# Performance work log

Measured on AMD Instinct MI355X. Metric: run time of the kernel, lower is better.

The kernel has to match this reference:

```python
import jax, jax.numpy as jnp
import numpy as np

B, S, R = 8, 4096, 512
E, K, ATOMS, XAR, TOPK = 64, 256, 16, 3, 2
TEMP = 1.0


def setup_inputs() -> dict:
    key = jax.random.key(0)
    k0, k1, k2, k3, k4 = jax.random.split(key, 5)
    x_latent = jax.random.normal(k0, (B, S, R), jnp.float32)
    router_w = jax.random.normal(k1, (E, R), jnp.float32) * (1.0 / np.sqrt(R))
    atoms = jax.random.normal(k2, (E, ATOMS, R), jnp.float32) * 0.01
    combo_weights = jax.random.uniform(k3, (E, K, XAR), jnp.float32) * 0.5 + 0.25
    combo_logits = jax.random.normal(k4, (E, K, XAR, ATOMS), jnp.float32) * 0.01
    return {"x_latent": x_latent, "router_w": router_w, "atoms": atoms,
            "combo_weights": combo_weights, "combo_logits": combo_logits}


def _expert_centroids(atoms, combo_weights, combo_logits):
    # Hard codeword path (vectorized over experts):
    # sign atoms -> pick argmax atom per (k, xor slot) -> weight -> sum -> sign -> mean over k
    binary = jnp.sign(atoms)                                   # [E, A, R]
    # softmax(logits/t) then argmax == argmax(logits) (monotone)
    idx = jnp.argmax(combo_logits, axis=-1)                    # [E, K, XAR]
    sel = binary[jnp.arange(E)[:, None, None], idx]            # [E, K, XAR, R]
    codewords = jnp.sign((sel * combo_weights[..., None]).sum(axis=2))  # [E, K, R]
    return codewords.mean(axis=1)                              # [E, R]


def reference(x_latent, router_w, atoms, combo_weights, combo_logits):
    t = max(TEMP, 0.1)
    router_logits = jnp.einsum('bsr,er->bse', x_latent, router_w)   # [B, S, E]
    probs_t = jax.nn.softmax(router_logits / t, axis=-1)
    gates, expert_ids = jax.lax.top_k(probs_t, TOPK)                # [B, S, 2]
    gates = gates / gates.sum(axis=-1, keepdims=True)

    centroids = _expert_centroids(atoms, combo_weights, combo_logits)  # [E, R]

    # aux load-balancing loss (uses untempered softmax)
    router_prob = jax.nn.softmax(router_logits, axis=-1)
    aux_loss = E * jnp.sum(router_prob.mean(axis=(0, 1)) *
                           (router_prob > 0).astype(x_latent.dtype).mean(axis=(0, 1)))

    # dense per-expert gate = sum over topk slots of gate * (id == e), then combine with centroids
    dense_gates = (jax.nn.one_hot(expert_ids, E, dtype=gates.dtype) *
                   gates[..., None]).sum(axis=-2)                    # [B, S, E]
    combined = jnp.einsum('bse,er->bsr', dense_gates, centroids)     # [B, S, R]
    return combined, aux_loss
```

## Files before the change

kernel.cpp:

```cpp
#include <hip/hip_runtime.h>
#include <math.h>

#define TOKENS 32768
#define RDIM 512
#define NEXP 64
#define NK 256
#define LDQ 136
#define PSTR 67
#define TAU 4.0e-3f

typedef unsigned short u16;
typedef float f32x4 __attribute__((ext_vector_type(4)));
typedef short s16x8 __attribute__((ext_vector_type(8)));

#define MFMA_B16(a, b, c) __builtin_amdgcn_mfma_f32_16x16x32_bf16(a, b, c, 0, 0, 0)

__device__ __forceinline__ void split_pack(float4 v, unsigned& h01, unsigned& h23,
                                           unsigned& l01, unsigned& l23) {
    unsigned u0 = __float_as_uint(v.x), u1 = __float_as_uint(v.y);
    unsigned u2 = __float_as_uint(v.z), u3 = __float_as_uint(v.w);
    float r0 = v.x - __uint_as_float(u0 & 0xFFFF0000u);
    float r1 = v.y - __uint_as_float(u1 & 0xFFFF0000u);
    float r2 = v.z - __uint_as_float(u2 & 0xFFFF0000u);
    float r3 = v.w - __uint_as_float(u3 & 0xFFFF0000u);
    h01 = (u0 >> 16) | (u1 & 0xFFFF0000u);
    h23 = (u2 >> 16) | (u3 & 0xFFFF0000u);
    l01 = (__float_as_uint(r0) >> 16) | (__float_as_uint(r1) & 0xFFFF0000u);
    l23 = (__float_as_uint(r2) >> 16) | (__float_as_uint(r3) & 0xFFFF0000u);
}

__device__ __forceinline__ void split8(float4 a, float4 b, s16x8& hi, s16x8& lo) {
    union U { unsigned u[4]; s16x8 v; };
    U H, L;
    split_pack(a, H.u[0], H.u[1], L.u[0], L.u[1]);
    split_pack(b, H.u[2], H.u[3], L.u[2], L.u[3]);
    hi = H.v; lo = L.v;
}

__global__ __launch_bounds__(256) void centroid_kernel(
    const float* __restrict__ atoms,
    const float* __restrict__ cw,
    const float* __restrict__ cl,
    float* __restrict__ cent,
    float* __restrict__ aux_sum,
    unsigned* __restrict__ aux_cnt)
{
    __shared__ unsigned pack[NK];
    const int e    = blockIdx.x >> 1;
    const int half = blockIdx.x & 1;
    const int tid  = threadIdx.x;

    if (blockIdx.x == 0 && tid < 64) { aux_sum[tid] = 0.f; aux_cnt[tid] = 0u; }

    {
        const int k = tid;
        unsigned u = 0;
        float w3[3];
        #pragma unroll
        for (int xx = 0; xx < 3; ++xx) {
            const float* cp = cl + ((((size_t)e * NK + k) * 3 + xx) << 4);
            float v[16];
            *(float4*)(v + 0)  = *(const float4*)(cp + 0);
            *(float4*)(v + 4)  = *(const float4*)(cp + 4);
            *(float4*)(v + 8)  = *(const float4*)(cp + 8);
            *(float4*)(v + 12) = *(const float4*)(cp + 12);
            float best = v[0]; int bi = 0;
            #pragma unroll
            for (int a = 1; a < 16; ++a) {
                if (v[a] > best) { best = v[a]; bi = a; }
            }
            u |= (unsigned)bi << (4 * xx);
            w3[xx] = cw[((size_t)e * NK + k) * 3 + xx];
        }
        unsigned lut = 0;
        #pragma unroll
        for (int c = 0; c < 8; ++c) {
            float val = ((c & 1) ? -w3[0] : w3[0])
                      + ((c & 2) ? -w3[1] : w3[1])
                      + ((c & 4) ? -w3[2] : w3[2]);
            lut |= (val < 0.f ? 1u : 0u) << c;
        }
        pack[k] = u | (lut << 16);
    }

    const int r = half * 256 + tid;
    unsigned B0 = 0;
    #pragma unroll
    for (int a = 0; a < 16; ++a)
        B0 |= (atoms[((size_t)e * 16 + a) * RDIM + r] < 0.f ? 1u : 0u) << a;
    __syncthreads();

    int n0 = 0;
    #pragma unroll 2
    for (int k = 0; k < NK; k += 8) {
        unsigned pk[8];
        #pragma unroll
        for (int j = 0; j < 8; ++j) pk[j] = pack[k + j];
        #pragma unroll
        for (int j = 0; j < 8; ++j) {
            unsigned u  = pk[j];
            unsigned i0 = u & 15u, i1 = (u >> 4) & 15u, i2 = (u >> 8) & 15u;
            unsigned c0 = ((B0 >> i0) & 1u) | (((B0 >> i1) & 1u) << 1) | (((B0 >> i2) & 1u) << 2);
            n0 += (u >> (16 + c0)) & 1u;
        }
    }
    cent[(size_t)e * RDIM + r] = 1.f - (float)n0 * (1.f / 128.f);
}

__global__ __launch_bounds__(256, 4) void moe_main(
    const float* __restrict__ x,
    const float* __restrict__ w,
    const float* __restrict__ cent,
    float* __restrict__ out,
    float* __restrict__ aux_sum,
    unsigned* __restrict__ aux_cnt)
{
    __shared__ u16 wlds[2 * 64 * LDQ];
    u16* whi = wlds;
    u16* wlo = wlds + 64 * LDQ;
    float* P     = (float*)wlds;
    float* candv = P + 64 * PSTR;
    int*   candi = (int*)(candv + 64 * 13);
    float* qsum  = (float*)(candi + 64 * 13);
    float* gateL = qsum + 64 * 5;
    __shared__ float s_aux[64];
    __shared__ unsigned s_cnt[64];

    const int tid  = threadIdx.x;
    const int lane = tid & 63;
    const int wave = tid >> 6;
    const int l15  = lane & 15;
    const int kgrp = (lane >> 4) << 3;
    const int tok0 = blockIdx.x * 64;

    if (tid < 64) { s_aux[tid] = 0.f; s_cnt[tid] = 0u; }

    f32x4 acc[4];
    #pragma unroll
    for (int nt = 0; nt < 4; ++nt) acc[nt] = (f32x4){0.f, 0.f, 0.f, 0.f};

    const float* xlane = x + (size_t)(tok0 + wave * 16 + l15) * RDIM + kgrp;
    const int wrow = tid >> 2;
    const int wseg = tid & 3;
    const float* wg = w + (size_t)wrow * RDIM + wseg * 32;
    const int woff = wrow * LDQ + wseg * 32;

    float4 preA[4], preB[4];
    #pragma unroll
    for (int i = 0; i < 4; ++i) {
        preA[i] = *(const float4*)(xlane + i * 32);
        preB[i] = *(const float4*)(xlane + i * 32 + 4);
    }

    #pragma unroll
    for (int q = 0; q < 4; ++q) {
        if (q) __syncthreads();
        {
            const float* wq = wg + q * 128;
            uint2 h2[2], l2[2];
            #pragma unroll
            for (int j = 0; j < 8; ++j) {
                float4 wv = *(const float4*)(wq + j * 4);
                split_pack(wv, h2[j & 1].x, h2[j & 1].y, l2[j & 1].x, l2[j & 1].y);
                if (j & 1) {
                    *(uint4*)&whi[woff + (j - 1) * 4] =
                        make_uint4(h2[0].x, h2[0].y, h2[1].x, h2[1].y);
                    *(uint4*)&wlo[woff + (j - 1) * 4] =
                        make_uint4(l2[0].x, l2[0].y, l2[1].x, l2[1].y);
                }
            }
        }
        __syncthreads();

        #pragma unroll
        for (int kb = 0; kb < 4; ++kb) {
            const int g = q * 4 + kb;
            s16x8 ah, al;
            split8(preA[g & 3], preB[g & 3], ah, al);
            if (g + 4 < 16) {
                const float* nx = xlane + (g + 4) * 32;
                preA[g & 3] = *(const float4*)(nx);
                preB[g & 3] = *(const float4*)(nx + 4);
            }
            const int kl = kb * 32 + kgrp;
            #pragma unroll
            for (int nt = 0; nt < 4; ++nt) {
                const int brow = nt * 16 + l15;
                s16x8 bh = *(const s16x8*)&whi[brow * LDQ + kl];
                s16x8 bl = *(const s16x8*)&wlo[brow * LDQ + kl];
                acc[nt] = MFMA_B16(ah, bh, acc[nt]);
                acc[nt] = MFMA_B16(ah, bl, acc[nt]);
                acc[nt] = MFMA_B16(al, bh, acc[nt]);
            }
        }
    }

    __syncthreads();
    #pragma unroll
    for (int nt = 0; nt < 4; ++nt)
        #pragma unroll
        for (int i = 0; i < 4; ++i)
            P[(wave * 16 + ((lane >> 4) << 2) + i) * PSTR + nt * 16 + l15] = acc[nt][i];
    __syncthreads();

    const int tt = tid & 63;
    const int ss = tid >> 6;
    float v[16];
    #pragma unroll
    for (int j = 0; j < 16; ++j) v[j] = P[tt * PSTR + ss * 16 + j];

    float m1 = -INFINITY, m2 = -INFINITY, m3 = -INFINITY;
    int   i1 = NEXP, i2 = NEXP, i3 = NEXP;
    #pragma unroll
    for (int j = 0; j < 16; ++j) {
        float val = v[j]; int e = ss * 16 + j;
        if (val > m1)      { m3 = m2; i3 = i2; m2 = m1; i2 = i1; m1 = val; i1 = e; }
        else if (val > m2) { m3 = m2; i3 = i2; m2 = val; i2 = e; }
        else if (val > m3) { m3 = val; i3 = e; }
    }
    candv[tt * 13 + ss * 3 + 0] = m1; candi[tt * 13 + ss * 3 + 0] = i1;
    candv[tt * 13 + ss * 3 + 1] = m2; candi[tt * 13 + ss * 3 + 1] = i2;
    candv[tt * 13 + ss * 3 + 2] = m3; candi[tt * 13 + ss * 3 + 2] = i3;
    __syncthreads();

    m1 = m2 = m3 = -INFINITY; i1 = i2 = i3 = NEXP;
    #pragma unroll
    for (int q = 0; q < 12; ++q) {
        float val = candv[tt * 13 + q]; int e = candi[tt * 13 + q];
        if (val > m1)      { m3 = m2; i3 = i2; m2 = m1; i2 = i1; m1 = val; i1 = e; }
        else if (val > m2) { m3 = m2; i3 = i2; m2 = val; i2 = e; }
        else if (val > m3) { m3 = val; i3 = e; }
    }

    float ex[16]; float ps = 0.f;
    #pragma unroll
    for (int j = 0; j < 16; ++j) { ex[j] = __expf(v[j] - m1); ps += ex[j]; }
    qsum[tt * 5 + ss] = ps;

    if (ss == 0) {
        {
            const float ed  = __expf(m2 - m1);
            const float inv = 1.f / (1.f + ed);
            gateL[tt * 4 + 0] = inv;
            gateL[tt * 4 + 1] = ed * inv;
            ((int*)gateL)[tt * 4 + 2] = i1;
            ((int*)gateL)[tt * 4 + 3] = i2;
        }
        unsigned long long bmask = __ballot(m2 - m3 < TAU);
        while (bmask) {
            const int f = __ffsll(bmask) - 1;
            bmask &= bmask - 1;
            int id3[3];
            id3[0] = __shfl(i1, f); id3[1] = __shfl(i2, f); id3[2] = __shfl(i3, f);
            const float* xrow = x + (size_t)(tok0 + f) * RDIM + lane * 8;
            float4 a0 = *(const float4*)(xrow);
            float4 a1 = *(const float4*)(xrow + 4);
            float d[3];
            #pragma unroll
            for (int jj = 0; jj < 3; ++jj) {
                const float* wrow2 = w + (size_t)id3[jj] * RDIM + lane * 8;
                float4 b0 = *(const float4*)(wrow2);
                float4 b1 = *(const float4*)(wrow2 + 4);
                float p = a0.x * b0.x;
                p = fmaf(a0.y, b0.y, p); p = fmaf(a0.z, b0.z, p); p = fmaf(a0.w, b0.w, p);
                p = fmaf(a1.x, b1.x, p); p = fmaf(a1.y, b1.y, p);
                p = fmaf(a1.z, b1.z, p); p = fmaf(a1.w, b1.w, p);
                #pragma unroll
                for (int off = 32; off; off >>= 1) p += __shfl_xor(p, off);
                d[jj] = p;
            }
            int b = 0;
            if (d[1] > d[0] || (d[1] == d[0] && id3[1] < id3[0])) b = 1;
            if (d[2] > d[b] || (d[2] == d[b] && id3[2] < id3[b])) b = 2;
            int sec;
            if (b == 0)      sec = (d[1] > d[2] || (d[1] == d[2] && id3[1] < id3[2])) ? 1 : 2;
            else if (b == 1) sec = (d[0] > d[2] || (d[0] == d[2] && id3[0] < id3[2])) ? 0 : 2;
            else             sec = (d[0] > d[1] || (d[0] == d[1] && id3[0] < id3[1])) ? 0 : 1;
            if (lane == f) {
                const float ed  = __expf(d[sec] - d[b]);
                const float inv = 1.f / (1.f + ed);
                gateL[f * 4 + 0] = inv;
                gateL[f * 4 + 1] = ed * inv;
                ((int*)gateL)[f * 4 + 2] = id3[b];
                ((int*)gateL)[f * 4 + 3] = id3[sec];
            }
        }
    }
    __syncthreads();

    float Z = 0.f;
    #pragma unroll
    for (int k = 0; k < 4; ++k) Z += qsum[tt * 5 + k];
    const float invZ = 1.f / Z;
    #pragma unroll
    for (int j = 0; j < 16; ++j) P[tt * PSTR + ss * 16 + j] = ex[j] * invZ;
    __syncthreads();

    {
        const int e = tid & 63, tq = tid >> 6;
        float s = 0.f; unsigned cn = 0u;
        #pragma unroll
        for (int t = 0; t < 16; ++t) {
            float pv = P[(tq * 16 + t) * PSTR + e];
            s += pv; cn += (pv > 0.f) ? 1u : 0u;
        }
        atomicAdd(&s_aux[e], s);
        atomicAdd(&s_cnt[e], cn);
    }
    __syncthreads();
    if (tid < 64) {
        atomicAdd(aux_sum + tid, s_aux[tid]);
        atomicAdd(aux_cnt + tid, s_cnt[tid]);
    }

    {
        const int e = lane;
        #pragma unroll
        for (int s2 = 0; s2 < 16; ++s2) {
            const int t2 = wave * 16 + s2;
            float4 g4 = *(float4*)&gateL[t2 * 4];
            const float g1 = g4.x, g2 = g4.y;
            const int e1 = __float_as_int(g4.z), e2 = __float_as_int(g4.w);
            const float4* c1 = (const float4*)(cent + (size_t)e1 * RDIM);
            const float4* c2 = (const float4*)(cent + (size_t)e2 * RDIM);
            float4* op = (float4*)(out + (size_t)(tok0 + t2) * RDIM);
            float4 A0 = c1[e],      Bb0 = c2[e];
            float4 A1 = c1[e + 64], Bb1 = c2[e + 64];
            float4 o0, o1;
            o0.x = fmaf(g1, A0.x, g2 * Bb0.x); o0.y = fmaf(g1, A0.y, g2 * Bb0.y);
            o0.z = fmaf(g1, A0.z, g2 * Bb0.z); o0.w = fmaf(g1, A0.w, g2 * Bb0.w);
            o1.x = fmaf(g1, A1.x, g2 * Bb1.x); o1.y = fmaf(g1, A1.y, g2 * Bb1.y);
            o1.z = fmaf(g1, A1.z, g2 * Bb1.z); o1.w = fmaf(g1, A1.w, g2 * Bb1.w);
            op[e]      = o0;
            op[e + 64] = o1;
        }
    }
}

__global__ __launch_bounds__(64) void aux_kernel(
    const float* __restrict__ sums,
    const unsigned* __restrict__ cnts,
    float* __restrict__ out_aux)
{
    const int e = threadIdx.x;
    float v = (sums[e] * (1.f / (float)TOKENS)) * ((float)cnts[e] * (1.f / (float)TOKENS));
    #pragma unroll
    for (int off = 32; off; off >>= 1) v += __shfl_xor(v, off);
    if (e == 0) out_aux[0] = (float)NEXP * v;
}

extern "C" void kernel_launch(void* const* d_in, const int* in_sizes, int n_in,
                              void* d_out, int out_size, void* d_ws, size_t ws_size,
                              hipStream_t stream) {
    const float* x     = (const float*)d_in[0];
    const float* rw    = (const float*)d_in[1];
    const float* atoms = (const float*)d_in[2];
    const float* cwts  = (const float*)d_in[3];
    const float* clog  = (const float*)d_in[4];
    float* out = (float*)d_out;

    float*    aux_sum = (float*)d_ws;
    unsigned* aux_cnt = (unsigned*)((char*)d_ws + 256);
    float*    cent    = (float*)((char*)d_ws + 512);

    centroid_kernel<<<128, 256, 0, stream>>>(atoms, cwts, clog, cent, aux_sum, aux_cnt);
    moe_main<<<512, 256, 0, stream>>>(x, rw, cent, out, aux_sum, aux_cnt);
    aux_kernel<<<1, 64, 0, stream>>>(aux_sum, aux_cnt, out + (size_t)TOKENS * RDIM);
}
```

Measured before the change: 165.7 us.

## Pre-split router weights into MFMA fragment layout, add smaller-block fast path

Router weights are split into bf16 hi/lo once in a prep kernel, which runs alongside the centroid computation. They are stored in a layout that matches the MFMA B-fragment, so the main kernel loads them straight from global/L2 instead of re-splitting and staging them through LDS in every block. The main kernel now uses 128-thread blocks covering 32 tokens each, with a 1024-block grid and a smaller LDS footprint, which should allow higher occupancy and removes the per-quarter syncthreads. The fast path is chosen only when the workspace is large enough. It trades LDS reuse of the weights for repeated global/L2 reads of the packed weights.

Result: no change. 168.1 us (+1.4%).

```diff
diff --git a/kernel.cpp b/kernel.cpp
--- a/kernel.cpp
+++ b/kernel.cpp
@@ -37,21 +37,11 @@
     hi = H.v; lo = L.v;
 }
 
-__global__ __launch_bounds__(256) void centroid_kernel(
-    const float* __restrict__ atoms,
-    const float* __restrict__ cw,
-    const float* __restrict__ cl,
-    float* __restrict__ cent,
-    float* __restrict__ aux_sum,
-    unsigned* __restrict__ aux_cnt)
+__device__ __forceinline__ void centroid_body(
+    int e, int half, int tid,
+    const float* __restrict__ atoms, const float* __restrict__ cw,
+    const float* __restrict__ cl, float* __restrict__ cent, unsigned* pack)
 {
-    __shared__ unsigned pack[NK];
-    const int e    = blockIdx.x >> 1;
-    const int half = blockIdx.x & 1;
-    const int tid  = threadIdx.x;
-
-    if (blockIdx.x == 0 && tid < 64) { aux_sum[tid] = 0.f; aux_cnt[tid] = 0u; }
-
     {
         const int k = tid;
         unsigned u = 0;
@@ -93,18 +83,264 @@
     int n0 = 0;
     #pragma unroll 2
     for (int k = 0; k < NK; k += 8) {
-        unsigned pk[8];
-        #pragma unroll
-        for (int j = 0; j < 8; ++j) pk[j] = pack[k + j];
+        unsigned pk8[8];
+        #pragma unroll
+        for (int j = 0; j < 8; ++j) pk8[j] = pack[k + j];
         #pragma unroll
         for (int j = 0; j < 8; ++j) {
-            unsigned u  = pk[j];
+            unsigned u  = pk8[j];
             unsigned i0 = u & 15u, i1 = (u >> 4) & 15u, i2 = (u >> 8) & 15u;
             unsigned c0 = ((B0 >> i0) & 1u) | (((B0 >> i1) & 1u) << 1) | (((B0 >> i2) & 1u) << 2);
             n0 += (u >> (16 + c0)) & 1u;
         }
     }
     cent[(size_t)e * RDIM + r] = 1.f - (float)n0 * (1.f / 128.f);
+}
+
+__global__ __launch_bounds__(256) void centroid_pack_kernel(
+    const float* __restrict__ atoms,
+    const float* __restrict__ cw,
+    const float* __restrict__ cl,
+    const float* __restrict__ w,
+    float* __restrict__ cent,
+    u16* __restrict__ pk_hi,
+    u16* __restrict__ pk_lo,
+    float* __restrict__ aux_sum,
+    unsigned* __restrict__ aux_cnt)
+{
+    __shared__ unsigned pack[NK];
+    const int tid = threadIdx.x;
+    if (blockIdx.x == 0 && tid < 64) { aux_sum[tid] = 0.f; aux_cnt[tid] = 0u; }
+
+    if (blockIdx.x < 128) {
+        centroid_body(blockIdx.x >> 1, blockIdx.x & 1, tid, atoms, cw, cl, cent, pack);
+    } else {
+        const int gid = (blockIdx.x - 128) * 256 + tid;
+        const int row = gid >> 7;
+        const int k0  = (gid & 127) * 4;
+        const int g   = k0 >> 5, kg = (k0 >> 3) & 3, j = k0 & 7;
+        const int idx = ((g * 4 + kg) * 64 + row) * 8 + j;
+        float4 wv = *(const float4*)(w + (size_t)row * RDIM + k0);
+        unsigned h01, h23, l01, l23;
+        split_pack(wv, h01, h23, l01, l23);
+        *(uint2*)&pk_hi[idx] = make_uint2(h01, h23);
+        *(uint2*)&pk_lo[idx] = make_uint2(l01, l23);
+    }
+}
+
+__global__ __launch_bounds__(128, 4) void moe_fast(
+    const float* __restrict__ x,
+    const u16* __restrict__ pk_hi,
+    const u16* __restrict__ pk_lo,
+    const float* __restrict__ w,
+    const float* __restrict__ cent,
+    float* __restrict__ out,
+    float* __restrict__ aux_sum,
+    unsigned* __restrict__ aux_cnt)
+{
+    __shared__ float P[32 * PSTR];
+    __shared__ float candv[32 * 13];
+    __shared__ int   candi[32 * 13];
+    __shared__ float qsum[32 * 5];
+    __shared__ float gateL[32 * 4];
+    __shared__ float s_aux[64];
+    __shared__ unsigned s_cnt[64];
+
+    const int tid  = threadIdx.x;
+    const int lane = tid & 63;
+    const int wv   = tid >> 6;
+    const int l15  = lane & 15;
+    const int kq   = lane >> 4;
+    const int kgrp = kq << 3;
+    const int tok0 = blockIdx.x * 32;
+
+    if (tid < 64) { s_aux[tid] = 0.f; s_cnt[tid] = 0u; }
+
+    f32x4 acc[4];
+    #pragma unroll
+    for (int nt = 0; nt < 4; ++nt) acc[nt] = (f32x4){0.f, 0.f, 0.f, 0.f};
+
+    const float* xlane = x + (size_t)(tok0 + wv * 16 + l15) * RDIM + kgrp;
+    const int fbase = kq * 512 + l15 * 8;
+
+    float4 pA[2], pB[2];
+    pA[0] = *(const float4*)(xlane);      pB[0] = *(const float4*)(xlane + 4);
+    pA[1] = *(const float4*)(xlane + 32); pB[1] = *(const float4*)(xlane + 36);
+
+    #pragma unroll
+    for (int g = 0; g < 16; ++g) {
+        s16x8 ah, al;
+        split8(pA[g & 1], pB[g & 1], ah, al);
+        if (g + 2 < 16) {
+            const float* nx = xlane + (g + 2) * 32;
+            pA[g & 1] = *(const float4*)(nx);
+            pB[g & 1] = *(const float4*)(nx + 4);
+        }
+        const u16* ph = pk_hi + g * 2048 + fbase;
+        const u16* pl = pk_lo + g * 2048 + fbase;
+        #pragma unroll
+        for (int nt = 0; nt < 4; ++nt) {
+            s16x8 bh = *(const s16x8*)(ph + nt * 128);
+            s16x8 bl = *(const s16x8*)(pl + nt * 128);
+            acc[nt] = MFMA_B16(ah, bh, acc[nt]);
+            acc[nt] = MFMA_B16(ah, bl, acc[nt]);
+            acc[nt] = MFMA_B16(al, bh, acc[nt]);
+        }
+    }
+
+    #pragma unroll
+    for (int nt = 0; nt < 4; ++nt)
+        #pragma unroll
+        for (int i = 0; i < 4; ++i)
+            P[(wv * 16 + (kq << 2) + i) * PSTR + nt * 16 + l15] = acc[nt][i];
+    __syncthreads();
+
+    const int tt = tid & 31;
+    const int ss = tid >> 5;
+    float v[16];
+    #pragma unroll
+    for (int j = 0; j < 16; ++j) v[j] = P[tt * PSTR + ss * 16 + j];
+
+    float m1 = -INFINITY, m2 = -INFINITY, m3 = -INFINITY;
+    int   i1 = NEXP, i2 = NEXP, i3 = NEXP;
+    #pragma unroll
+    for (int j = 0; j < 16; ++j) {
+        float val = v[j]; int e = ss * 16 + j;
+        if (val > m1)      { m3 = m2; i3 = i2; m2 = m1; i2 = i1; m1 = val; i1 = e; }
+        else if (val > m2) { m3 = m2; i3 = i2; m2 = val; i2 = e; }
+        else if (val > m3) { m3 = val; i3 = e; }
+    }
+    candv[tt * 13 + ss * 3 + 0] = m1; candi[tt * 13 + ss * 3 + 0] = i1;
+    candv[tt * 13 + ss * 3 + 1] = m2; candi[tt * 13 + ss * 3 + 1] = i2;
+    candv[tt * 13 + ss * 3 + 2] = m3; candi[tt * 13 + ss * 3 + 2] = i3;
+    __syncthreads();
+
+    m1 = m2 = m3 = -INFINITY; i1 = i2 = i3 = NEXP;
+    #pragma unroll
+    for (int q = 0; q < 12; ++q) {
+        float val = candv[tt * 13 + q]; int e = candi[tt * 13 + q];
+        if (val > m1)      { m3 = m2; i3 = i2; m2 = m1; i2 = i1; m1 = val; i1 = e; }
+        else if (val > m2) { m3 = m2; i3 = i2; m2 = val; i2 = e; }
+        else if (val > m3) { m3 = val; i3 = e; }
+    }
+
+    float ex[16]; float ps = 0.f;
+    #pragma unroll
+    for (int j = 0; j < 16; ++j) { ex[j] = __expf(v[j] - m1); ps += ex[j]; }
+    qsum[tt * 5 + ss] = ps;
+
+    if (wv == 0) {
+        if (lane < 32) {
+            const float ed  = __expf(m2 - m1);
+            const float inv = 1.f / (1.f + ed);
+            gateL[tt * 4 + 0] = inv;
+            gateL[tt * 4 + 1] = ed * inv;
+            ((int*)gateL)[tt * 4 + 2] = i1;
+            ((int*)gateL)[tt * 4 + 3] = i2;
+        }
+        unsigned long long bmask = __ballot(lane < 32 && (m2 - m3 < TAU));
+        while (bmask) {
+            const int f = __ffsll(bmask) - 1;
+            bmask &= bmask - 1;
+            int id3[3];
+            id3[0] = __shfl(i1, f); id3[1] = __shfl(i2, f); id3[2] = __shfl(i3, f);
+            const float* xrow = x + (size_t)(tok0 + f) * RDIM + lane * 8;
+            float4 a0 = *(const float4*)(xrow);
+            float4 a1 = *(const float4*)(xrow + 4);
+            float d[3];
+            #pragma unroll
+            for (int jj = 0; jj < 3; ++jj) {
+                const float* wrow = w + (size_t)id3[jj] * RDIM + lane * 8;
+                float4 b0 = *(const float4*)(wrow);
+                float4 b1 = *(const float4*)(wrow + 4);
+                float p = a0.x * b0.x;
+                p = fmaf(a0.y, b0.y, p); p = fmaf(a0.z, b0.z, p); p = fmaf(a0.w, b0.w, p);
+                p = fmaf(a1.x, b1.x, p); p = fmaf(a1.y, b1.y, p);
+                p = fmaf(a1.z, b1.z, p); p = fmaf(a1.w, b1.w, p);
+                #pragma unroll
+                for (int off = 32; off; off >>= 1) p += __shfl_xor(p, off);
+                d[jj] = p;
+            }
+            int b = 0;
+            if (d[1] > d[0] || (d[1] == d[0] && id3[1] < id3[0])) b = 1;
+            if (d[2] > d[b] || (d[2] == d[b] && id3[2] < id3[b])) b = 2;
+            int sec;
+            if (b == 0)      sec = (d[1] > d[2] || (d[1] == d[2] && id3[1] < id3[2])) ? 1 : 2;
+            else if (b == 1) sec = (d[0] > d[2] || (d[0] == d[2] && id3[0] < id3[2])) ? 0 : 2;
+            else             sec = (d[0] > d[1] || (d[0] == d[1] && id3[0] < id3[1])) ? 0 : 1;
+            if (lane == f) {
+                const float ed  = __expf(d[sec] - d[b]);
+                const float inv = 1.f / (1.f + ed);
+                gateL[f * 4 + 0] = inv;
+                gateL[f * 4 + 1] = ed * inv;
+                ((int*)gateL)[f * 4 + 2] = id3[b];
+                ((int*)gateL)[f * 4 + 3] = id3[sec];
+            }
+        }
+    }
+    __syncthreads();
+
+    float Z = 0.f;
+    #pragma unroll
+    for (int k = 0; k < 4; ++k) Z += qsum[tt * 5 + k];
+    const float invZ = 1.f / Z;
+    #pragma unroll
+    for (int j = 0; j < 16; ++j) P[tt * PSTR + ss * 16 + j] = ex[j] * invZ;
+    __syncthreads();
+
+    {
+        const int e = tid & 63, tq = tid >> 6;
+        float s = 0.f; unsigned cn = 0u;
+        #pragma unroll
+        for (int t = 0; t < 16; ++t) {
+            float pv = P[(tq * 16 + t) * PSTR + e];
+            s += pv; cn += (pv > 0.f) ? 1u : 0u;
+        }
+        atomicAdd(&s_aux[e], s);
+        atomicAdd(&s_cnt[e], cn);
+    }
+    __syncthreads();
+    if (tid < 64) {
+        atomicAdd(aux_sum + tid, s_aux[tid]);
+        atomicAdd(aux_cnt + tid, s_cnt[tid]);
+    }
+
+    {
+        const int e = lane;
+        #pragma unroll
+        for (int s2 = 0; s2 < 16; ++s2) {
+            const int t2 = wv * 16 + s2;
+            float4 g4 = *(float4*)&gateL[t2 * 4];
+            const float g1 = g4.x, g2 = g4.y;
+            const int e1 = __float_as_int(g4.z), e2 = __float_as_int(g4.w);
+            const float4* c1 = (const float4*)(cent + (size_t)e1 * RDIM);
+            const float4* c2 = (const float4*)(cent + (size_t)e2 * RDIM);
+            float4* op = (float4*)(out + (size_t)(tok0 + t2) * RDIM);
+            float4 A0 = c1[e],      Bb0 = c2[e];
+            float4 A1 = c1[e + 64], Bb1 = c2[e + 64];
+            float4 o0, o1;
+            o0.x = fmaf(g1, A0.x, g2 * Bb0.x); o0.y = fmaf(g1, A0.y, g2 * Bb0.y);
+            o0.z = fmaf(g1, A0.z, g2 * Bb0.z); o0.w = fmaf(g1, A0.w, g2 * Bb0.w);
+            o1.x = fmaf(g1, A1.x, g2 * Bb1.x); o1.y = fmaf(g1, A1.y, g2 * Bb1.y);
+            o1.z = fmaf(g1, A1.z, g2 * Bb1.z); o1.w = fmaf(g1, A1.w, g2 * Bb1.w);
+            op[e]      = o0;
+            op[e + 64] = o1;
+        }
+    }
+}
+
+__global__ __launch_bounds__(256) void centroid_kernel(
+    const float* __restrict__ atoms,
+    const float* __restrict__ cw,
+    const float* __restrict__ cl,
+    float* __restrict__ cent,
+    float* __restrict__ aux_sum,
+    unsigned* __restrict__ aux_cnt)
+{
+    __shared__ unsigned pack[NK];
+    const int tid = threadIdx.x;
+    if (blockIdx.x == 0 && tid < 64) { aux_sum[tid] = 0.f; aux_cnt[tid] = 0u; }
+    centroid_body(blockIdx.x >> 1, blockIdx.x & 1, tid, atoms, cw, cl, cent, pack);
 }
 
 __global__ __launch_bounds__(256, 4) void moe_main(
@@ -160,8 +396,8 @@
             uint2 h2[2], l2[2];
             #pragma unroll
             for (int j = 0; j < 8; ++j) {
-                float4 wv = *(const float4*)(wq + j * 4);
-                split_pack(wv, h2[j & 1].x, h2[j & 1].y, l2[j & 1].x, l2[j & 1].y);
+                float4 wvv = *(const float4*)(wq + j * 4);
+                split_pack(wvv, h2[j & 1].x, h2[j & 1].y, l2[j & 1].x, l2[j & 1].y);
                 if (j & 1) {
                     *(uint4*)&whi[woff + (j - 1) * 4] =
                         make_uint4(h2[0].x, h2[0].y, h2[1].x, h2[1].y);
@@ -358,12 +594,22 @@
     const float* cwts  = (const float*)d_in[3];
     const float* clog  = (const float*)d_in[4];
     float* out = (float*)d_out;
+    float* out_aux = out + (size_t)TOKENS * RDIM;
 
     float*    aux_sum = (float*)d_ws;
     unsigned* aux_cnt = (unsigned*)((char*)d_ws + 256);
     float*    cent    = (float*)((char*)d_ws + 512);
-
-    centroid_kernel<<<128, 256, 0, stream>>>(atoms, cwts, clog, cent, aux_sum, aux_cnt);
-    moe_main<<<512, 256, 0, stream>>>(x, rw, cent, out, aux_sum, aux_cnt);
-    aux_kernel<<<1, 64, 0, stream>>>(aux_sum, aux_cnt, out + (size_t)TOKENS * RDIM);
-}
+    u16*      pk_hi   = (u16*)((char*)d_ws + 512 + 131072);
+    u16*      pk_lo   = (u16*)((char*)d_ws + 512 + 131072 + 65536);
+    const bool fast = ws_size >= (size_t)(512 + 131072 + 2 * 65536);
+
+    if (fast) {
+        centroid_pack_kernel<<<160, 256, 0, stream>>>(atoms, cwts, clog, rw, cent,
+                                                      pk_hi, pk_lo, aux_sum, aux_cnt);
+        moe_fast<<<1024, 128, 0, stream>>>(x, pk_hi, pk_lo, rw, cent, out, aux_sum, aux_cnt);
+    } else {
+        centroid_kernel<<<128, 256, 0, stream>>>(atoms, cwts, clog, cent, aux_sum, aux_cnt);
+        moe_main<<<512, 256, 0, stream>>>(x, rw, cent, out, aux_sum, aux_cnt);
+    }
+    aux_kernel<<<1, 64, 0, stream>>>(aux_sum, aux_cnt, out_aux);
+}
```
